# Kernel optimization log

Hardware: AMD Instinct MI355X
Metric: run time of the kernel (lower is better)

The kernel has to match this reference:

```python
import jax, jax.numpy as jnp
import numpy as np

N_NODES = 50000
N_EDGES = 800000
NODE_IN, EDGE_IN, EFT, OUT = 128, 64, 32, 64


def setup_inputs() -> dict:
    key = jax.random.key(0)
    ks = jax.random.split(key, 8)
    h = jax.random.normal(ks[0], (N_NODES, NODE_IN), dtype=jnp.float32)
    edge_feat = jax.random.normal(ks[1], (N_EDGES, EDGE_IN), dtype=jnp.float32)
    src = jax.random.randint(ks[2], (N_EDGES,), 0, N_NODES, dtype=jnp.int32)
    dst = jax.random.randint(ks[3], (N_EDGES,), 0, N_NODES, dtype=jnp.int32)
    Wn = jax.random.normal(ks[4], (OUT, NODE_IN), dtype=jnp.float32) * 0.05
    We = jax.random.normal(ks[5], (EFT, EDGE_IN), dtype=jnp.float32) * 0.05
    Wa = jax.random.normal(ks[6], (1, OUT + EFT + OUT), dtype=jnp.float32) * 0.05
    W2 = jax.random.normal(ks[7], (OUT, OUT + EFT), dtype=jnp.float32) * 0.05
    return {"h": h, "edge_feat": edge_feat, "src": src, "dst": dst,
            "Wn": Wn, "We": We, "Wa": Wa, "W2": W2}


def reference(h, edge_feat, src, dst, Wn, We, Wa, W2):
    N = h.shape[0]
    # node / edge feature projections (bias=False linears)
    z = h @ Wn.T                       # [N, OUT]
    ef = edge_feat @ We.T              # [E, EFT]
    # per-edge message: concat(src node ft, edge ft)
    zne = jnp.concatenate([z[src], ef], axis=1)            # [E, OUT+EFT]
    # attention logit: leaky_relu(attn_fc([zne, z_dst]))
    a = jnp.concatenate([zne, z[dst]], axis=1) @ Wa.T      # [E, 1]
    s = jax.nn.leaky_relu(a[:, 0], negative_slope=0.01)    # [E]
    # segment softmax over incoming edges of each dst node
    seg_max = jax.ops.segment_max(s, dst, num_segments=N)
    ex = jnp.exp(s - seg_max[dst])
    denom = jax.ops.segment_sum(ex, dst, num_segments=N)
    alpha = ex / denom[dst]                                # [E]
    # weighted scatter-sum aggregation, then fc2
    agg = jax.ops.segment_sum(alpha[:, None] * zne, dst, num_segments=N)
    h_new = agg @ W2.T                                     # [N, OUT]
    # DGL semantics: nodes with no incoming messages keep ndata['z'] = fc_n(h)
    deg = jax.ops.segment_sum(jnp.ones_like(s), dst, num_segments=N)
    return jnp.where((deg > 0)[:, None], h_new, z)
```

## Files before the change

kernel.cpp:

```cpp
#include <hip/hip_runtime.h>
#include <math.h>

#define N_NODES 50000
#define N_EDGES 800000
#define NB1 196

typedef __attribute__((ext_vector_type(8))) short bf16x8;
typedef __attribute__((ext_vector_type(4))) float f32x4;

__device__ __forceinline__ unsigned short f2bf(float f) {
    unsigned u = __float_as_uint(f);
    unsigned r = (u + 0x7FFFu + ((u >> 16) & 1u)) >> 16;
    return (unsigned short)r;
}
__device__ __forceinline__ float bf2f(unsigned short u) {
    return __uint_as_float(((unsigned)u) << 16);
}
__device__ __forceinline__ unsigned pack2bf(float a, float b) {
    return (unsigned)f2bf(a) | ((unsigned)f2bf(b) << 16);
}

__global__ __launch_bounds__(256) void kw_kernel(const float* __restrict__ We,
                                                 const float* __restrict__ Wa,
                                                 const float* __restrict__ Wn,
                                                 const float* __restrict__ W2,
                                                 short* __restrict__ Bpack,
                                                 int* __restrict__ degi) {
    int t = blockIdx.x * 256 + threadIdx.x;
    if (t < N_NODES) degi[t] = 0;
    if (t < 34 * 512) {
        int f = t >> 9, u = t & 511, lane = u >> 3, j = u & 7;
        int c = lane & 15, G = lane >> 4;
        float v = 0.f;
        if (f < 8) {
            int s = f >> 2, n = f & 3;
            int kp = 32 * s + 8 * G + j;
            #pragma unroll
            for (int kk = 0; kk < 32; ++kk)
                v += W2[(16 * n + c) * 96 + 64 + kk] * We[kk * 64 + kp];
        } else if (f < 10) {
            int s = f - 8;
            if (c == 0) {
                int kp = 32 * s + 8 * G + j;
                #pragma unroll
                for (int jj = 0; jj < 32; ++jj) v += Wa[64 + jj] * We[jj * 64 + kp];
            }
        } else if (f < 26) {
            int qf = f - 10, s = qf >> 2, n = qf & 3;
            v = Wn[(16 * n + c) * 128 + 32 * s + 8 * G + j];
        } else {
            int qf = f - 26, s = qf >> 2, n = qf & 3;
            v = W2[(16 * n + c) * 96 + 32 * s + 8 * G + j];
        }
        Bpack[t] = (short)f2bf(v);
    }
}

__global__ __launch_bounds__(256) void node_hist_kernel(
    const float* __restrict__ h, const float* __restrict__ Wa,
    const short* __restrict__ Bpack, const int* __restrict__ dst,
    float* __restrict__ z, ushort4* __restrict__ y16p,
    float* __restrict__ asrc, float* __restrict__ adst,
    int* __restrict__ degi, int* __restrict__ ranks)
{
    __shared__ float zl[4][1088];
    int t = threadIdx.x;
    if (blockIdx.x >= 782) {
        int e = (blockIdx.x - 782) * 256 + t;
        if (e < N_EDGES) ranks[e] = atomicAdd(&degi[dst[e]], 1);
        return;
    }
    int w = t >> 6, l = t & 63, c = l & 15, G = l >> 4;
    int T = blockIdx.x * 4 + w;
    if (T >= 3125) return;
    int n0 = T * 16;
    const bf16x8* Bp = (const bf16x8*)Bpack;

    const float* hp = h + (size_t)(n0 + c) * 128 + 8 * G;
    bf16x8 a[4];
    #pragma unroll
    for (int s = 0; s < 4; ++s) {
        float4 lo = *(const float4*)(hp + 32 * s);
        float4 hi = *(const float4*)(hp + 32 * s + 4);
        a[s][0] = (short)f2bf(lo.x); a[s][1] = (short)f2bf(lo.y);
        a[s][2] = (short)f2bf(lo.z); a[s][3] = (short)f2bf(lo.w);
        a[s][4] = (short)f2bf(hi.x); a[s][5] = (short)f2bf(hi.y);
        a[s][6] = (short)f2bf(hi.z); a[s][7] = (short)f2bf(hi.w);
    }
    f32x4 acc[4] = {{0.f,0.f,0.f,0.f},{0.f,0.f,0.f,0.f},{0.f,0.f,0.f,0.f},{0.f,0.f,0.f,0.f}};
    #pragma unroll
    for (int n = 0; n < 4; ++n)
        #pragma unroll
        for (int s = 0; s < 4; ++s)
            acc[n] = __builtin_amdgcn_mfma_f32_16x16x32_bf16(a[s], Bp[(10 + 4*s + n)*64 + l], acc[n], 0, 0, 0);

    float was[4], wad[4];
    #pragma unroll
    for (int n = 0; n < 4; ++n) { was[n] = Wa[16*n + c]; wad[n] = Wa[96 + 16*n + c]; }

    #pragma unroll
    for (int r = 0; r < 4; ++r) {
        int row = n0 + 4 * G + r;
        #pragma unroll
        for (int n = 0; n < 4; ++n) {
            z[(size_t)row * 64 + 16 * n + c] = acc[n][r];
            zl[w][(4 * G + r) * 68 + 16 * n + c] = acc[n][r];
        }
        float ps = acc[0][r]*was[0] + acc[1][r]*was[1] + acc[2][r]*was[2] + acc[3][r]*was[3];
        float pd = acc[0][r]*wad[0] + acc[1][r]*wad[1] + acc[2][r]*wad[2] + acc[3][r]*wad[3];
        ps += __shfl_xor(ps, 1); ps += __shfl_xor(ps, 2);
        ps += __shfl_xor(ps, 4); ps += __shfl_xor(ps, 8);
        pd += __shfl_xor(pd, 1); pd += __shfl_xor(pd, 2);
        pd += __shfl_xor(pd, 4); pd += __shfl_xor(pd, 8);
        if (c == 0) { asrc[row] = ps; adst[row] = pd; }
    }

    bf16x8 ay[2];
    #pragma unroll
    for (int s = 0; s < 2; ++s)
        #pragma unroll
        for (int j = 0; j < 8; ++j)
            ay[s][j] = (short)f2bf(zl[w][c * 68 + 32 * s + 8 * G + j]);
    f32x4 accy[4] = {{0.f,0.f,0.f,0.f},{0.f,0.f,0.f,0.f},{0.f,0.f,0.f,0.f},{0.f,0.f,0.f,0.f}};
    #pragma unroll
    for (int n = 0; n < 4; ++n)
        #pragma unroll
        for (int s = 0; s < 2; ++s)
            accy[n] = __builtin_amdgcn_mfma_f32_16x16x32_bf16(ay[s], Bp[(26 + 4*s + n)*64 + l], accy[n], 0, 0, 0);
    #pragma unroll
    for (int r = 0; r < 4; ++r) {
        ushort4 yo;
        yo.x = f2bf(accy[0][r]); yo.y = f2bf(accy[1][r]);
        yo.z = f2bf(accy[2][r]); yo.w = f2bf(accy[3][r]);
        y16p[(size_t)(n0 + 4 * G + r) * 16 + c] = yo;
    }
}

__global__ __launch_bounds__(256) void scan1_kernel(const int* __restrict__ degi,
                                                    int* __restrict__ partial) {
    int t = threadIdx.x, i = blockIdx.x * 256 + t;
    int d = (i < N_NODES) ? degi[i] : 0;
    #pragma unroll
    for (int off = 32; off; off >>= 1) d += __shfl_down(d, off);
    __shared__ int wsum[4];
    if ((t & 63) == 0) wsum[t >> 6] = d;
    __syncthreads();
    if (t == 0) partial[blockIdx.x] = wsum[0] + wsum[1] + wsum[2] + wsum[3];
}

__global__ __launch_bounds__(256) void scan2_kernel(int* __restrict__ partial) {
    __shared__ int s[256];
    int t = threadIdx.x;
    int v = (t < NB1) ? partial[t] : 0;
    s[t] = v; __syncthreads();
    for (int off = 1; off < 256; off <<= 1) {
        int x = (t >= off) ? s[t - off] : 0;
        __syncthreads();
        s[t] += x;
        __syncthreads();
    }
    if (t < NB1) partial[t] = s[t] - v;
}

__global__ __launch_bounds__(256) void scan3_kernel(const int* __restrict__ degi,
                                                    const int* __restrict__ partial,
                                                    int* __restrict__ start) {
    __shared__ int s[256];
    int t = threadIdx.x, i = blockIdx.x * 256 + t;
    int d = (i < N_NODES) ? degi[i] : 0;
    s[t] = d; __syncthreads();
    for (int off = 1; off < 256; off <<= 1) {
        int x = (t >= off) ? s[t - off] : 0;
        __syncthreads();
        s[t] += x;
        __syncthreads();
    }
    if (i < N_NODES) start[i] = partial[blockIdx.x] + s[t] - d;
}

__global__ __launch_bounds__(256, 2) void edge_kernel(
    const float* __restrict__ edge_feat, const int* __restrict__ src,
    const int* __restrict__ dst, const int* __restrict__ ranks,
    const int* __restrict__ start, const float* __restrict__ asrc,
    const float* __restrict__ adst, const short* __restrict__ Bpack,
    const ushort4* __restrict__ y16p,
    unsigned short* __restrict__ wout, float* __restrict__ exslot)
{
    int t = threadIdx.x, w = t >> 6, l = t & 63;
    int c = l & 15, G = l >> 4;
    int wbase = blockIdx.x * 256 + w * 64;

    const bf16x8* Bp = (const bf16x8*)Bpack;
    bf16x8 bc[8];
    #pragma unroll
    for (int f = 0; f < 8; ++f) bc[f] = Bp[f * 64 + l];
    bf16x8 b2a = Bp[8 * 64 + l];
    bf16x8 b2b = Bp[9 * 64 + l];

    int e = wbase + l;
    int se = src[e];
    int de = dst[e];
    int slot = start[de] + ranks[e];
    float apre = asrc[se] + adst[de];

    const float* efr = edge_feat + (size_t)(wbase + c) * 64 + G * 8;
    float4 n0 = *(const float4*)(efr);
    float4 n1 = *(const float4*)(efr + 4);
    float4 n2 = *(const float4*)(efr + 32);
    float4 n3 = *(const float4*)(efr + 36);

    #pragma unroll
    for (int k = 0; k < 4; ++k) {
        float4 c0 = n0, c1 = n1, c2 = n2, c3 = n3;
        if (k < 3) {
            const float* efn = edge_feat + (size_t)(wbase + 16 * (k + 1) + c) * 64 + G * 8;
            n0 = *(const float4*)(efn);
            n1 = *(const float4*)(efn + 4);
            n2 = *(const float4*)(efn + 32);
            n3 = *(const float4*)(efn + 36);
        }
        int sr[4], sl4[4]; float ap[4];
        #pragma unroll
        for (int r = 0; r < 4; ++r) {
            int si = 16 * k + 4 * G + r;
            sr[r]  = __shfl(se, si);
            sl4[r] = __shfl(slot, si);
            ap[r]  = __shfl(apre, si);
        }
        ushort4 yv[4];
        #pragma unroll
        for (int r = 0; r < 4; ++r) yv[r] = y16p[(size_t)sr[r] * 16 + c];

        bf16x8 a0, a1;
        a0[0] = (short)f2bf(c0.x); a0[1] = (short)f2bf(c0.y);
        a0[2] = (short)f2bf(c0.z); a0[3] = (short)f2bf(c0.w);
        a0[4] = (short)f2bf(c1.x); a0[5] = (short)f2bf(c1.y);
        a0[6] = (short)f2bf(c1.z); a0[7] = (short)f2bf(c1.w);
        a1[0] = (short)f2bf(c2.x); a1[1] = (short)f2bf(c2.y);
        a1[2] = (short)f2bf(c2.z); a1[3] = (short)f2bf(c2.w);
        a1[4] = (short)f2bf(c3.x); a1[5] = (short)f2bf(c3.y);
        a1[6] = (short)f2bf(c3.z); a1[7] = (short)f2bf(c3.w);

        f32x4 acc[4] = {{0.f,0.f,0.f,0.f},{0.f,0.f,0.f,0.f},{0.f,0.f,0.f,0.f},{0.f,0.f,0.f,0.f}};
        f32x4 acc2 = {0.f, 0.f, 0.f, 0.f};
        #pragma unroll
        for (int n = 0; n < 4; ++n) {
            acc[n] = __builtin_amdgcn_mfma_f32_16x16x32_bf16(a0, bc[n], acc[n], 0, 0, 0);
            acc[n] = __builtin_amdgcn_mfma_f32_16x16x32_bf16(a1, bc[4 + n], acc[n], 0, 0, 0);
        }
        acc2 = __builtin_amdgcn_mfma_f32_16x16x32_bf16(a0, b2a, acc2, 0, 0, 0);
        acc2 = __builtin_amdgcn_mfma_f32_16x16x32_bf16(a1, b2b, acc2, 0, 0, 0);

        #pragma unroll
        for (int r = 0; r < 4; ++r) {
            float u0 = acc[0][r] + bf2f(yv[r].x);
            float u1 = acc[1][r] + bf2f(yv[r].y);
            float u2 = acc[2][r] + bf2f(yv[r].z);
            float u3 = acc[3][r] + bf2f(yv[r].w);
            uint2 o;
            o.x = pack2bf(u0, u1);
            o.y = pack2bf(u2, u3);
            *(uint2*)&wout[(size_t)sl4[r] * 64 + 4 * c] = o;
            if (c == 0) {
                float aa = ap[r] + acc2[r];
                float sg = aa > 0.f ? aa : 0.01f * aa;
                exslot[sl4[r]] = __expf(sg);
            }
        }
    }
}

__global__ __launch_bounds__(256) void agg_kernel(
    const unsigned short* __restrict__ wout, const float* __restrict__ exslot,
    const int* __restrict__ start, const int* __restrict__ degi,
    const float* __restrict__ z, float* __restrict__ out)
{
    int t = threadIdx.x, w = t >> 6, l = t & 63;
    int d    = blockIdx.x * 4 + w;
    int base = __builtin_amdgcn_readfirstlane(start[d]);
    int deg  = __builtin_amdgcn_readfirstlane(degi[d]);
    const unsigned short* wp = wout + (size_t)base * 64 + l;
    const float* xp = exslot + base;

    float acc = 0.f, den = 0.f;
    for (int i = 0; i < deg; i += 8) {
        #pragma unroll
        for (int j = 0; j < 8; ++j) {
            int idx = i + j;
            bool vld = idx < deg;
            int ic = vld ? idx : deg - 1;
            unsigned short v = wp[(size_t)ic * 64];
            float x = vld ? xp[ic] : 0.f;
            acc += x * bf2f(v);
            den += x;
        }
    }

    int comp = 16 * (l & 3) + (l >> 2);
    if (deg > 0)
        out[(size_t)d * 64 + comp] = acc / den;
    else
        out[(size_t)d * 64 + comp] = z[(size_t)d * 64 + comp];
}

extern "C" void kernel_launch(void* const* d_in, const int* in_sizes, int n_in,
                              void* d_out, int out_size, void* d_ws, size_t ws_size,
                              hipStream_t stream) {
    const float* h         = (const float*)d_in[0];
    const float* edge_feat = (const float*)d_in[1];
    const int*   src       = (const int*)d_in[2];
    const int*   dst       = (const int*)d_in[3];
    const float* Wn        = (const float*)d_in[4];
    const float* We        = (const float*)d_in[5];
    const float* Wa        = (const float*)d_in[6];
    const float* W2        = (const float*)d_in[7];
    float* out = (float*)d_out;

    char* p = (char*)d_ws;
    unsigned short* wout   = (unsigned short*)p; p += (size_t)N_EDGES * 64 * 2;
    float*          z      = (float*)p;          p += (size_t)N_NODES * 64 * 4;
    ushort4*        y16p   = (ushort4*)p;        p += (size_t)N_NODES * 64 * 2;
    float*          exslot = (float*)p;          p += (size_t)N_EDGES * 4;
    float*          asrc   = (float*)p;          p += (size_t)N_NODES * 4;
    float*          adst   = (float*)p;          p += (size_t)N_NODES * 4;
    int*            degi   = (int*)p;            p += (size_t)N_NODES * 4;
    int*            start  = (int*)p;            p += (size_t)N_NODES * 4;
    int*            ranks  = (int*)p;            p += (size_t)N_EDGES * 4;
    int*            partial= (int*)p;            p += (size_t)256 * 4;
    short*          Bpack  = (short*)p;          p += (size_t)34 * 512 * 2;

    kw_kernel<<<NB1, 256, 0, stream>>>(We, Wa, Wn, W2, Bpack, degi);
    node_hist_kernel<<<782 + 3125, 256, 0, stream>>>(h, Wa, Bpack, dst, z, y16p,
                                                     asrc, adst, degi, ranks);
    scan1_kernel<<<NB1, 256, 0, stream>>>(degi, partial);
    scan2_kernel<<<1, 256, 0, stream>>>(partial);
    scan3_kernel<<<NB1, 256, 0, stream>>>(degi, partial, start);
    edge_kernel<<<3125, 256, 0, stream>>>(edge_feat, src, dst, ranks, start,
                                          asrc, adst, Bpack, y16p, wout, exslot);
    agg_kernel<<<N_NODES / 4, 256, 0, stream>>>(wout, exslot, start, degi, z, out);
}
```

Baseline: 169.2 us.

## Fuse three-pass scan into decoupled look-back scan and vectorize aggregation loads

Replaces the three scan kernels with one single-pass scan that uses decoupled look-back via per-block flags and aggregates in global memory, which removes two kernel launches. The flags are reset in kw_kernel. The aggregation kernel now has each lane load a ushort4 of four features for one of four edges, handling eight edges per iteration, and then reduces across lane groups with shuffles. This trades per-lane scalar loads for wider loads at the cost of a cross-lane reduction. The look-back spin assumes earlier blocks are already resident, which holds for 196 blocks on this GPU.

```diff
diff --git a/kernel.cpp b/kernel.cpp
--- a/kernel.cpp
+++ b/kernel.cpp
@@ -25,9 +25,11 @@
                                                  const float* __restrict__ Wn,
                                                  const float* __restrict__ W2,
                                                  short* __restrict__ Bpack,
-                                                 int* __restrict__ degi) {
+                                                 int* __restrict__ degi,
+                                                 int* __restrict__ sFlag) {
     int t = blockIdx.x * 256 + threadIdx.x;
     if (t < N_NODES) degi[t] = 0;
+    if (t < 256) sFlag[t] = 0;
     if (t < 34 * 512) {
         int f = t >> 9, u = t & 511, lane = u >> 3, j = u & 7;
         int c = lane & 15, G = lane >> 4;
@@ -136,37 +138,13 @@
     }
 }
 
-__global__ __launch_bounds__(256) void scan1_kernel(const int* __restrict__ degi,
-                                                    int* __restrict__ partial) {
-    int t = threadIdx.x, i = blockIdx.x * 256 + t;
-    int d = (i < N_NODES) ? degi[i] : 0;
-    #pragma unroll
-    for (int off = 32; off; off >>= 1) d += __shfl_down(d, off);
-    __shared__ int wsum[4];
-    if ((t & 63) == 0) wsum[t >> 6] = d;
-    __syncthreads();
-    if (t == 0) partial[blockIdx.x] = wsum[0] + wsum[1] + wsum[2] + wsum[3];
-}
-
-__global__ __launch_bounds__(256) void scan2_kernel(int* __restrict__ partial) {
+__global__ __launch_bounds__(256) void scan_fused_kernel(
+    const int* __restrict__ degi, int* __restrict__ start,
+    int* __restrict__ sAgg, int* __restrict__ sPref, int* __restrict__ sFlag)
+{
     __shared__ int s[256];
-    int t = threadIdx.x;
-    int v = (t < NB1) ? partial[t] : 0;
-    s[t] = v; __syncthreads();
-    for (int off = 1; off < 256; off <<= 1) {
-        int x = (t >= off) ? s[t - off] : 0;
-        __syncthreads();
-        s[t] += x;
-        __syncthreads();
-    }
-    if (t < NB1) partial[t] = s[t] - v;
-}
-
-__global__ __launch_bounds__(256) void scan3_kernel(const int* __restrict__ degi,
-                                                    const int* __restrict__ partial,
-                                                    int* __restrict__ start) {
-    __shared__ int s[256];
-    int t = threadIdx.x, i = blockIdx.x * 256 + t;
+    __shared__ int exc_s;
+    int b = blockIdx.x, t = threadIdx.x, i = b * 256 + t;
     int d = (i < N_NODES) ? degi[i] : 0;
     s[t] = d; __syncthreads();
     for (int off = 1; off < 256; off <<= 1) {
@@ -175,7 +153,34 @@
         s[t] += x;
         __syncthreads();
     }
-    if (i < N_NODES) start[i] = partial[blockIdx.x] + s[t] - d;
+    int incl = s[t];
+    int bsum = s[255];
+    if (t == 0) {
+        if (b == 0) {
+            __hip_atomic_store(&sPref[0], bsum, __ATOMIC_RELEASE, __HIP_MEMORY_SCOPE_AGENT);
+            __hip_atomic_store(&sFlag[0], 2, __ATOMIC_RELEASE, __HIP_MEMORY_SCOPE_AGENT);
+            exc_s = 0;
+        } else {
+            __hip_atomic_store(&sAgg[b], bsum, __ATOMIC_RELEASE, __HIP_MEMORY_SCOPE_AGENT);
+            __hip_atomic_store(&sFlag[b], 1, __ATOMIC_RELEASE, __HIP_MEMORY_SCOPE_AGENT);
+            int run = 0, j = b - 1;
+            while (true) {
+                int f;
+                do { f = __hip_atomic_load(&sFlag[j], __ATOMIC_ACQUIRE, __HIP_MEMORY_SCOPE_AGENT); } while (f == 0);
+                if (f == 2) {
+                    run += __hip_atomic_load(&sPref[j], __ATOMIC_ACQUIRE, __HIP_MEMORY_SCOPE_AGENT);
+                    break;
+                }
+                run += __hip_atomic_load(&sAgg[j], __ATOMIC_ACQUIRE, __HIP_MEMORY_SCOPE_AGENT);
+                --j;
+            }
+            __hip_atomic_store(&sPref[b], run + bsum, __ATOMIC_RELEASE, __HIP_MEMORY_SCOPE_AGENT);
+            __hip_atomic_store(&sFlag[b], 2, __ATOMIC_RELEASE, __HIP_MEMORY_SCOPE_AGENT);
+            exc_s = run;
+        }
+    }
+    __syncthreads();
+    if (i < N_NODES) start[i] = exc_s + incl - d;
 }
 
 __global__ __launch_bounds__(256, 2) void edge_kernel(
@@ -271,36 +276,54 @@
 }
 
 __global__ __launch_bounds__(256) void agg_kernel(
-    const unsigned short* __restrict__ wout, const float* __restrict__ exslot,
+    const ushort4* __restrict__ wout4, const float* __restrict__ exslot,
     const int* __restrict__ start, const int* __restrict__ degi,
     const float* __restrict__ z, float* __restrict__ out)
 {
-    int t = threadIdx.x, w = t >> 6, l = t & 63;
+    int t = threadIdx.x, w = t >> 6, l = t & 63, c = l & 15, g = l >> 4;
     int d    = blockIdx.x * 4 + w;
     int base = __builtin_amdgcn_readfirstlane(start[d]);
     int deg  = __builtin_amdgcn_readfirstlane(degi[d]);
-    const unsigned short* wp = wout + (size_t)base * 64 + l;
-    const float* xp = exslot + base;
-
-    float acc = 0.f, den = 0.f;
+
+    float4 acc = make_float4(0.f, 0.f, 0.f, 0.f);
+    float den = 0.f;
     for (int i = 0; i < deg; i += 8) {
-        #pragma unroll
-        for (int j = 0; j < 8; ++j) {
-            int idx = i + j;
-            bool vld = idx < deg;
-            int ic = vld ? idx : deg - 1;
-            unsigned short v = wp[(size_t)ic * 64];
-            float x = vld ? xp[ic] : 0.f;
-            acc += x * bf2f(v);
-            den += x;
-        }
-    }
-
-    int comp = 16 * (l & 3) + (l >> 2);
-    if (deg > 0)
-        out[(size_t)d * 64 + comp] = acc / den;
-    else
-        out[(size_t)d * 64 + comp] = z[(size_t)d * 64 + comp];
+        int i0 = i + g, i1 = i + 4 + g;
+        bool v0 = i0 < deg, v1 = i1 < deg;
+        int k0 = v0 ? i0 : 0, k1 = v1 ? i1 : 0;
+        ushort4 ua = wout4[(size_t)(base + k0) * 16 + c];
+        ushort4 ub = wout4[(size_t)(base + k1) * 16 + c];
+        float xa = v0 ? exslot[base + i0] : 0.f;
+        float xb = v1 ? exslot[base + i1] : 0.f;
+        acc.x += xa * bf2f(ua.x); acc.y += xa * bf2f(ua.y);
+        acc.z += xa * bf2f(ua.z); acc.w += xa * bf2f(ua.w);
+        den += xa;
+        acc.x += xb * bf2f(ub.x); acc.y += xb * bf2f(ub.y);
+        acc.z += xb * bf2f(ub.z); acc.w += xb * bf2f(ub.w);
+        den += xb;
+    }
+
+    acc.x += __shfl_xor(acc.x, 16); acc.x += __shfl_xor(acc.x, 32);
+    acc.y += __shfl_xor(acc.y, 16); acc.y += __shfl_xor(acc.y, 32);
+    acc.z += __shfl_xor(acc.z, 16); acc.z += __shfl_xor(acc.z, 32);
+    acc.w += __shfl_xor(acc.w, 16); acc.w += __shfl_xor(acc.w, 32);
+    den += __shfl_xor(den, 16); den += __shfl_xor(den, 32);
+
+    if (g == 0) {
+        size_t ob = (size_t)d * 64;
+        if (deg > 0) {
+            float inv = 1.f / den;
+            out[ob + c]      = acc.x * inv;
+            out[ob + 16 + c] = acc.y * inv;
+            out[ob + 32 + c] = acc.z * inv;
+            out[ob + 48 + c] = acc.w * inv;
+        } else {
+            out[ob + c]      = z[ob + c];
+            out[ob + 16 + c] = z[ob + 16 + c];
+            out[ob + 32 + c] = z[ob + 32 + c];
+            out[ob + 48 + c] = z[ob + 48 + c];
+        }
+    }
 }
 
 extern "C" void kernel_launch(void* const* d_in, const int* in_sizes, int n_in,
@@ -326,16 +349,17 @@
     int*            degi   = (int*)p;            p += (size_t)N_NODES * 4;
     int*            start  = (int*)p;            p += (size_t)N_NODES * 4;
     int*            ranks  = (int*)p;            p += (size_t)N_EDGES * 4;
-    int*            partial= (int*)p;            p += (size_t)256 * 4;
+    int*            sAgg   = (int*)p;            p += (size_t)256 * 4;
+    int*            sPref  = (int*)p;            p += (size_t)256 * 4;
+    int*            sFlag  = (int*)p;            p += (size_t)256 * 4;
     short*          Bpack  = (short*)p;          p += (size_t)34 * 512 * 2;
 
-    kw_kernel<<<NB1, 256, 0, stream>>>(We, Wa, Wn, W2, Bpack, degi);
+    kw_kernel<<<NB1, 256, 0, stream>>>(We, Wa, Wn, W2, Bpack, degi, sFlag);
     node_hist_kernel<<<782 + 3125, 256, 0, stream>>>(h, Wa, Bpack, dst, z, y16p,
                                                      asrc, adst, degi, ranks);
-    scan1_kernel<<<NB1, 256, 0, stream>>>(degi, partial);
-    scan2_kernel<<<1, 256, 0, stream>>>(partial);
-    scan3_kernel<<<NB1, 256, 0, stream>>>(degi, partial, start);
+    scan_fused_kernel<<<NB1, 256, 0, stream>>>(degi, start, sAgg, sPref, sFlag);
     edge_kernel<<<3125, 256, 0, stream>>>(edge_feat, src, dst, ranks, start,
                                           asrc, adst, Bpack, y16p, wout, exslot);
-    agg_kernel<<<N_NODES / 4, 256, 0, stream>>>(wout, exslot, start, degi, z, out);
-}
+    agg_kernel<<<N_NODES / 4, 256, 0, stream>>>((const ushort4*)wout, exslot,
+                                                start, degi, z, out);
+}
```

Result: slower. 231.5 us (+36.8%).
